# Kernel tuning notes

Hardware: AMD Instinct MI355X
Metric: run time of the kernel (lower is better)

The kernel has to match this reference:

```python
import jax, jax.numpy as jnp
import numpy as np

N = 50000
E = 1600000
IN, HID, OUT = 32, 64, 64

def setup_inputs() -> dict:
    key = jax.random.key(0)
    ks = jax.random.split(key, 10)
    x1 = jax.random.normal(ks[0], (N, IN), dtype=jnp.float32)
    x2 = jax.random.normal(ks[1], (N, IN), dtype=jnp.float32)
    ei1 = jax.random.randint(ks[2], (2, E), 0, N, dtype=jnp.int64)
    ei2 = jax.random.randint(ks[3], (2, E), 0, N, dtype=jnp.int64)
    s1 = 1.0 / np.sqrt(2 * IN)
    s2 = 1.0 / np.sqrt(2 * HID)
    W1 = jax.random.uniform(ks[4], (2 * IN, HID), jnp.float32, -s1, s1)
    b1 = jax.random.uniform(ks[5], (HID,), jnp.float32, -s1, s1)
    prelu_a = jnp.full((HID,), 0.25, dtype=jnp.float32)  # PReLU per-channel init
    W2 = jax.random.uniform(ks[6], (2 * HID, OUT), jnp.float32, -s2, s2)
    b2 = jax.random.uniform(ks[7], (OUT,), jnp.float32, -s2, s2)
    return {"x1": x1, "edge_index1": ei1, "x2": x2, "edge_index2": ei2,
            "W1": W1, "b1": b1, "prelu_a": prelu_a, "W2": W2, "b2": b2}

def _edge_conv(x, src, dst, W, b, n_nodes):
    # PyG EdgeConv: msg = MLP([x_i, x_j - x_i]), aggr = max over incoming edges
    xi = x[dst]                     # [E, d] target node feats
    xj = x[src]                     # [E, d] source node feats
    msg = jax.nn.relu(jnp.concatenate([xi, xj - xi], axis=-1) @ W + b)  # [E, out]
    agg = jax.ops.segment_max(msg, dst, num_segments=n_nodes)
    return jnp.where(jnp.isfinite(agg), agg, 0.0)  # nodes with no in-edges -> 0

def _prelu(x, a):
    return jnp.where(x >= 0, x, a * x)

def _embed(x, edge_index, W1, b1, prelu_a, W2, b2):
    src, dst = edge_index[0], edge_index[1]
    h = _prelu(_edge_conv(x, src, dst, W1, b1, x.shape[0]), prelu_a)
    return _edge_conv(h, src, dst, W2, b2, x.shape[0])

def reference(x1, edge_index1, x2, edge_index2, W1, b1, prelu_a, W2, b2):
    e1 = _embed(x1, edge_index1, W1, b1, prelu_a, W2, b2)
    e2 = _embed(x2, edge_index2, W1, b1, prelu_a, W2, b2)
    return (e1, e2)
```

## Files before the change

### kernel.cpp

```cpp
#include <hip/hip_runtime.h>
#include <hip/hip_fp16.h>


constexpr int HID   = 64;
constexpr int TILE  = 32;
constexpr int TSH   = 5;
constexpr int CAP   = 2048;
constexpr int MAXNB = 2048;
constexpr int EPT   = 16;
constexpr int CAPN  = 96;

typedef _Float16 half8 __attribute__((ext_vector_type(8)));
typedef float    f32x4 __attribute__((ext_vector_type(4)));

__device__ __forceinline__ unsigned int pkmax(unsigned int a, unsigned int b) {
    unsigned int d;
    asm("v_pk_max_f16 %0, %1, %2" : "=v"(d) : "v"(a), "v"(b));
    return d;
}
__device__ __forceinline__ unsigned int f2hbits(float f) {
    const __half h = __float2half_rn(f);
    return (unsigned int)*reinterpret_cast<const unsigned short*>(&h);
}
__device__ __forceinline__ float h2f(unsigned int b16) {
    const unsigned short b = (unsigned short)b16;
    __half h;
    *reinterpret_cast<unsigned short*>(&h) = b;
    return __half2float(h);
}

struct G {
    const float* x;
    const int*   src;
    const int*   dst;
    int* bcnt;
    unsigned int* bin;
    float*          u;
    unsigned short* vk;
    float*          out;
};

__global__ __launch_bounds__(256) void prep_w_kernel(
    const float* __restrict__ W1, const float* __restrict__ W2,
    _Float16* __restrict__ Wc1, _Float16* __restrict__ Wc2)
{
    const int i = blockIdx.x * 256 + threadIdx.x;
    if (i < 32 * 64) {
        const int k = i >> 6, c = i & 63;
        const float lo = W1[k * 64 + c], hi = W1[(32 + k) * 64 + c];
        Wc1[k * 128 + c]      = (_Float16)(lo - hi);
        Wc1[k * 128 + 64 + c] = (_Float16)hi;
    }
    const int j = i - 32 * 64;
    if (j >= 0 && j < 64 * 64) {
        const int k = j >> 6, c = j & 63;
        const float lo = W2[k * 64 + c], hi = W2[(64 + k) * 64 + c];
        Wc2[k * 128 + c]      = (_Float16)(lo - hi);
        Wc2[k * 128 + 64 + c] = (_Float16)hi;
    }
}

__global__ __launch_bounds__(256) void bin_kernel(G g0, G g1, int E, int NB) {
    const G g = blockIdx.y ? g1 : g0;
    __shared__ int lh[MAXNB];
    __shared__ int lb[MAXNB];
    for (int i = threadIdx.x; i < NB; i += 256) lh[i] = 0;
    __syncthreads();

    const int base = blockIdx.x * 256 * EPT;
    unsigned int rec[EPT];
    int bb[EPT];
    #pragma unroll
    for (int k = 0; k < EPT; ++k) {
        const int i = base + k * 256 + threadIdx.x;
        if (i < E) {
            const int d = g.dst[i];
            const int s = g.src[i];
            rec[k] = ((unsigned int)s << TSH) | (unsigned int)(d & (TILE - 1));
            bb[k]  = d >> TSH;
            atomicAdd(&lh[bb[k]], 1);
        } else bb[k] = -1;
    }
    __syncthreads();
    for (int t = threadIdx.x; t < NB; t += 256) {
        const int c = lh[t];
        lb[t] = c ? atomicAdd(&g.bcnt[t], c) : 0;
        lh[t] = 0;
    }
    __syncthreads();
    #pragma unroll
    for (int k = 0; k < EPT; ++k) {
        if (bb[k] >= 0) {
            const int off = atomicAdd(&lh[bb[k]], 1);
            const int pos = lb[bb[k]] + off;
            if (pos < CAP)
                g.bin[(size_t)bb[k] * CAP + pos] = rec[k];
        }
    }
}

template<int K>
__global__ __launch_bounds__(256) void gemm_mfma_kernel(
    G g0, G g1, const _Float16* __restrict__ Wc,
    const float* __restrict__ bias, int N)
{
    const G g = blockIdx.y ? g1 : g0;
    constexpr int KH = K / 32;
    const int lane = threadIdx.x & 63;
    const int m    = lane & 15;
    const int quad = lane >> 4;
    const int wid  = (blockIdx.x * 256 + threadIdx.x) >> 6;
    const int nW   = (gridDim.x * 256) >> 6;

    half8 bf[8][KH];
    #pragma unroll
    for (int t = 0; t < 8; ++t)
        #pragma unroll
        for (int h = 0; h < KH; ++h)
            #pragma unroll
            for (int j = 0; j < 8; ++j)
                bf[t][h][j] = Wc[(h * 32 + quad * 8 + j) * 128 + t * 16 + m];

    float bv[4];
    #pragma unroll
    for (int t = 0; t < 4; ++t) bv[t] = bias[t * 16 + m];

    const float* __restrict__ inp = (K == 32) ? g.x : g.out;
    const int tiles = (N + 15) / 16;

    for (int tile = wid; tile < tiles; tile += nW) {
        const int nbase = tile * 16;
        const int nodeA = min(nbase + m, N - 1);
        const float4* rp = (const float4*)(inp + (size_t)nodeA * K);

        half8 a[KH];
        #pragma unroll
        for (int h = 0; h < KH; ++h) {
            const float4 f0 = rp[h * 8 + quad * 2];
            const float4 f1 = rp[h * 8 + quad * 2 + 1];
            a[h][0] = (_Float16)f0.x; a[h][1] = (_Float16)f0.y;
            a[h][2] = (_Float16)f0.z; a[h][3] = (_Float16)f0.w;
            a[h][4] = (_Float16)f1.x; a[h][5] = (_Float16)f1.y;
            a[h][6] = (_Float16)f1.z; a[h][7] = (_Float16)f1.w;
        }

        f32x4 acc[8];
        #pragma unroll
        for (int t = 0; t < 8; ++t) {
            acc[t] = (f32x4){0.f, 0.f, 0.f, 0.f};
            #pragma unroll
            for (int h = 0; h < KH; ++h)
                acc[t] = __builtin_amdgcn_mfma_f32_16x16x32_f16(
                    a[h], bf[t][h], acc[t], 0, 0, 0);
        }

        #pragma unroll
        for (int r = 0; r < 4; ++r) {
            const int node = nbase + quad * 4 + r;
            if (node < N) {
                float* urow = g.u + (size_t)node * HID;
                #pragma unroll
                for (int t = 0; t < 4; ++t)
                    urow[t * 16 + m] = acc[t][r] + bv[t];
                const unsigned int e0 = f2hbits(acc[4][r]);
                const unsigned int e1 = f2hbits(acc[5][r]);
                const unsigned int e2 = f2hbits(acc[6][r]);
                const unsigned int e3 = f2hbits(acc[7][r]);
                uint2 pack;
                pack.x = (e1 << 16) | e0;
                pack.y = (e3 << 16) | e2;
                ((uint2*)(g.vk + (size_t)node * HID))[m] = pack;
            }
        }
    }
}

__global__ __launch_bounds__(256) void agg_kernel(G g0, G g1, int N, int NB, int two) {
    int b, gi;
    if (two) {
        const int bid = blockIdx.x;
        const int xcd = bid & 7;
        gi = xcd >> 2;
        b  = (bid >> 3) * 4 + (xcd & 3);
    } else { gi = 0; b = blockIdx.x; }
    if (b >= NB) return;
    const G g = gi ? g1 : g0;

    __shared__ int lcnt[TILE];
    __shared__ unsigned short lrec[TILE][CAPN];
    for (int i = threadIdx.x; i < TILE; i += 256) lcnt[i] = 0;
    __syncthreads();

    const int cnt = min(g.bcnt[b], CAP);
    const unsigned int* __restrict__ bp = g.bin + (size_t)b * CAP;
    for (int i = threadIdx.x; i < cnt; i += 256) {
        const unsigned int rec = bp[i];
        const int d = rec & (TILE - 1);
        const int p = atomicAdd(&lcnt[d], 1);
        if (p < CAPN) lrec[d][p] = (unsigned short)(rec >> TSH);
    }
    __syncthreads();

    const int grp = threadIdx.x >> 4;
    const int sub = threadIdx.x & 15;
    const uint2* __restrict__ vk2 = (const uint2*)g.vk;

    #pragma unroll
    for (int half = 0; half < 2; ++half) {
        const int nl = grp + half * 16;
        const int n  = b * TILE + nl;
        if (n >= N) continue;
        const int c = min(lcnt[nl], CAPN);

        unsigned int m0 = 0xFC00FC00u, m1 = 0xFC00FC00u;
        int j = 0;
        for (; j + 8 <= c; j += 8) {
            const uint4 rq = *(const uint4*)(&lrec[nl][j]);
            unsigned int s[8];
            s[0] = rq.x & 0xFFFFu; s[1] = rq.x >> 16;
            s[2] = rq.y & 0xFFFFu; s[3] = rq.y >> 16;
            s[4] = rq.z & 0xFFFFu; s[5] = rq.z >> 16;
            s[6] = rq.w & 0xFFFFu; s[7] = rq.w >> 16;
            uint2 a[8];
            #pragma unroll
            for (int k = 0; k < 8; ++k) a[k] = vk2[(size_t)s[k] * 16 + sub];
            #pragma unroll
            for (int k = 0; k < 8; ++k) {
                m0 = pkmax(m0, a[k].x);
                m1 = pkmax(m1, a[k].y);
            }
        }
        for (; j < c; ++j) {
            const uint2 a = vk2[(size_t)lrec[nl][j] * 16 + sub];
            m0 = pkmax(m0, a.x);
            m1 = pkmax(m1, a.y);
        }

        float mv[4];
        mv[0] = h2f(m0 & 0xFFFFu); mv[1] = h2f(m0 >> 16);
        mv[2] = h2f(m1 & 0xFFFFu); mv[3] = h2f(m1 >> 16);

        const float* __restrict__ urow = g.u + (size_t)n * HID;
        float* __restrict__ orow = g.out + (size_t)n * HID;
        #pragma unroll
        for (int t = 0; t < 4; ++t) {
            float r = 0.f;
            if (c > 0) r = fmaxf(urow[sub + 16 * t] + mv[t], 0.f);
            orow[sub + 16 * t] = r;
        }
    }
}


extern "C" void kernel_launch(void* const* d_in, const int* in_sizes, int n_in,
                              void* d_out, int out_size, void* d_ws, size_t ws_size,
                              hipStream_t stream) {
    const float* x1  = (const float*)d_in[0];
    const int*   ei1 = (const int*)d_in[1];
    const float* x2  = (const float*)d_in[2];
    const int*   ei2 = (const int*)d_in[3];
    const float* W1  = (const float*)d_in[4];
    const float* b1  = (const float*)d_in[5];
    const float* W2  = (const float*)d_in[7];
    const float* b2  = (const float*)d_in[8];

    const int N  = in_sizes[0] / 32;
    const int E  = in_sizes[1] / 2;
    const int NB = (N + TILE - 1) / TILE;
    float* out = (float*)d_out;

    const size_t rowB = (size_t)N * HID * sizeof(float);
    const size_t vkB  = ((size_t)N * HID * 2 + 63) & ~(size_t)63;
    const size_t binB = ((size_t)NB * CAP * sizeof(int) + 63) & ~(size_t)63;
    const size_t nbB  = ((size_t)(NB + 2) * sizeof(int) + 63) & ~(size_t)63;
    const size_t wc1B = ((size_t)32 * 128 * 2 + 63) & ~(size_t)63;
    const size_t wc2B = ((size_t)64 * 128 * 2 + 63) & ~(size_t)63;

    const int bBlk = (E + 256 * EPT - 1) / (256 * EPT);
    const int gBlk = 256;
    const int pBlk = (32 * 64 + 64 * 64 + 255) / 256;
    const int aggBlk2 = ((NB + 3) / 4) * 8;

    _Float16* wc1 = nullptr;
    _Float16* wc2 = nullptr;

    auto run = [&](G ga, G gb, int ny) {
        hipMemsetAsync(ga.bcnt, 0, (size_t)ny * nbB, stream);
        bin_kernel <<<dim3(bBlk, ny), 256, 0, stream>>>(ga, gb, E, NB);
        gemm_mfma_kernel<32><<<dim3(gBlk, ny), 256, 0, stream>>>(ga, gb, wc1, b1, N);
        if (ny == 2) agg_kernel<<<aggBlk2, 256, 0, stream>>>(ga, gb, N, NB, 1);
        else         agg_kernel<<<NB,      256, 0, stream>>>(ga, ga, N, NB, 0);
        gemm_mfma_kernel<64><<<dim3(gBlk, ny), 256, 0, stream>>>(ga, gb, wc2, b2, N);
        if (ny == 2) agg_kernel<<<aggBlk2, 256, 0, stream>>>(ga, gb, N, NB, 1);
        else         agg_kernel<<<NB,      256, 0, stream>>>(ga, ga, N, NB, 0);
    };

    char* ws = (char*)d_ws;
    const size_t needBoth = 2 * rowB + 2 * vkB + 2 * binB + 2 * nbB + wc1B + wc2B;

    if (ws_size >= needBoth) {
        float* u0 = (float*)ws;                  ws += rowB;
        float* u1 = (float*)ws;                  ws += rowB;
        unsigned int* bin0 = (unsigned int*)ws;  ws += binB;
        unsigned int* bin1 = (unsigned int*)ws;  ws += binB;
        unsigned short* vk0 = (unsigned short*)ws;  ws += vkB;
        unsigned short* vk1 = (unsigned short*)ws;  ws += vkB;
        wc1 = (_Float16*)ws;                     ws += wc1B;
        wc2 = (_Float16*)ws;                     ws += wc2B;
        int* bcnt0 = (int*)ws;                   ws += nbB;
        int* bcnt1 = (int*)ws;

        G g0{x1, ei1, ei1 + E, bcnt0, bin0, u0, vk0, out};
        G g1{x2, ei2, ei2 + E, bcnt1, bin1, u1, vk1, out + (size_t)N * HID};
        prep_w_kernel<<<pBlk, 256, 0, stream>>>(W1, W2, wc1, wc2);
        run(g0, g1, 2);
    } else {
        float* u = (float*)ws;                   ws += rowB;
        unsigned int* bin = (unsigned int*)ws;   ws += binB;
        unsigned short* vk = (unsigned short*)ws;  ws += vkB;
        wc1 = (_Float16*)ws;                     ws += wc1B;
        wc2 = (_Float16*)ws;                     ws += wc2B;
        int* bcnt = (int*)ws;

        prep_w_kernel<<<pBlk, 256, 0, stream>>>(W1, W2, wc1, wc2);
        for (int g = 0; g < 2; ++g) {
            const int* ei = g ? ei2 : ei1;
            G gp{g ? x2 : x1, ei, ei + E, bcnt, bin,
                 u, vk, out + (size_t)g * N * HID};
            run(gp, gp, 1);
        }
    }
}
```

Measured before the change: 249.2 us.

## Widen agg tiles to 128 nodes with sentinel-padded edge lists and split halves

The node tile grows from 32 to 128 per block, and bin capacity and the number of buckets change to match. Each node's incoming edge list is padded to a multiple of 8 using a sentinel row N, which prep_w_kernel fills with -inf fp16, so the scalar tail loop is gone. Each 8-lane group now handles four nodes in two passes, one per column half, which raises loads in flight per thread. The cost is larger shared-memory tiles, extra gathers of the sentinel row, and fewer, heavier blocks. It also relies on N fitting in 16 bits and on CAP=5120 being enough per 128-node bin.

Measured after the change: 299.7 us. +20.3%, slower.

```diff
diff --git a/kernel.cpp b/kernel.cpp
--- a/kernel.cpp
+++ b/kernel.cpp
@@ -3,10 +3,10 @@
 
 
 constexpr int HID   = 64;
-constexpr int TILE  = 32;
-constexpr int TSH   = 5;
-constexpr int CAP   = 2048;
-constexpr int MAXNB = 2048;
+constexpr int TILE  = 128;
+constexpr int TSH   = 7;
+constexpr int CAP   = 5120;
+constexpr int MAXNB = 512;
 constexpr int EPT   = 16;
 constexpr int CAPN  = 96;
 
@@ -42,7 +42,8 @@
 
 __global__ __launch_bounds__(256) void prep_w_kernel(
     const float* __restrict__ W1, const float* __restrict__ W2,
-    _Float16* __restrict__ Wc1, _Float16* __restrict__ Wc2)
+    _Float16* __restrict__ Wc1, _Float16* __restrict__ Wc2,
+    unsigned short* __restrict__ vkS0, unsigned short* __restrict__ vkS1, int N)
 {
     const int i = blockIdx.x * 256 + threadIdx.x;
     if (i < 32 * 64) {
@@ -57,6 +58,11 @@
         const float lo = W2[k * 64 + c], hi = W2[(64 + k) * 64 + c];
         Wc2[k * 128 + c]      = (_Float16)(lo - hi);
         Wc2[k * 128 + 64 + c] = (_Float16)hi;
+    }
+    const int q = i - (32 * 64 + 64 * 64);
+    if (q >= 0 && q < 2 * HID) {
+        if (q < HID) vkS0[(size_t)N * HID + q]       = 0xFC00u;
+        else         vkS1[(size_t)N * HID + (q-HID)] = 0xFC00u;
     }
 }
 
@@ -200,21 +206,27 @@
         if (p < CAPN) lrec[d][p] = (unsigned short)(rec >> TSH);
     }
     __syncthreads();
-
-    const int grp = threadIdx.x >> 4;
-    const int sub = threadIdx.x & 15;
+    for (int t = threadIdx.x; t < TILE; t += 256) {
+        const int c  = min(lcnt[t], CAPN);
+        const int cp = (c + 7) & ~7;
+        for (int p = c; p < cp; ++p) lrec[t][p] = (unsigned short)N;
+        lcnt[t] = cp;
+    }
+    __syncthreads();
+
+    const int grp = threadIdx.x >> 3;
+    const int sub = threadIdx.x & 7;
     const uint2* __restrict__ vk2 = (const uint2*)g.vk;
 
-    #pragma unroll
-    for (int half = 0; half < 2; ++half) {
-        const int nl = grp + half * 16;
-        const int n  = b * TILE + nl;
-        if (n >= N) continue;
-        const int c = min(lcnt[nl], CAPN);
-
+    unsigned int mA[4][2], mB[4][2];
+    int cp4[4];
+
+    #pragma unroll
+    for (int i = 0; i < 4; ++i) {
+        const int nl = grp + 32 * i;
+        cp4[i] = lcnt[nl];
         unsigned int m0 = 0xFC00FC00u, m1 = 0xFC00FC00u;
-        int j = 0;
-        for (; j + 8 <= c; j += 8) {
+        for (int j = 0; j < cp4[i]; j += 8) {
             const uint4 rq = *(const uint4*)(&lrec[nl][j]);
             unsigned int s[8];
             s[0] = rq.x & 0xFFFFu; s[1] = rq.x >> 16;
@@ -230,24 +242,47 @@
                 m1 = pkmax(m1, a[k].y);
             }
         }
-        for (; j < c; ++j) {
-            const uint2 a = vk2[(size_t)lrec[nl][j] * 16 + sub];
-            m0 = pkmax(m0, a.x);
-            m1 = pkmax(m1, a.y);
-        }
-
-        float mv[4];
-        mv[0] = h2f(m0 & 0xFFFFu); mv[1] = h2f(m0 >> 16);
-        mv[2] = h2f(m1 & 0xFFFFu); mv[3] = h2f(m1 >> 16);
-
+        mA[i][0] = m0; mA[i][1] = m1;
+    }
+
+    #pragma unroll
+    for (int i = 0; i < 4; ++i) {
+        const int nl = grp + 32 * i;
+        unsigned int m0 = 0xFC00FC00u, m1 = 0xFC00FC00u;
+        for (int j = 0; j < cp4[i]; j += 8) {
+            const uint4 rq = *(const uint4*)(&lrec[nl][j]);
+            unsigned int s[8];
+            s[0] = rq.x & 0xFFFFu; s[1] = rq.x >> 16;
+            s[2] = rq.y & 0xFFFFu; s[3] = rq.y >> 16;
+            s[4] = rq.z & 0xFFFFu; s[5] = rq.z >> 16;
+            s[6] = rq.w & 0xFFFFu; s[7] = rq.w >> 16;
+            uint2 a[8];
+            #pragma unroll
+            for (int k = 0; k < 8; ++k) a[k] = vk2[(size_t)s[k] * 16 + 8 + sub];
+            #pragma unroll
+            for (int k = 0; k < 8; ++k) {
+                m0 = pkmax(m0, a[k].x);
+                m1 = pkmax(m1, a[k].y);
+            }
+        }
+        mB[i][0] = m0; mB[i][1] = m1;
+    }
+
+    #pragma unroll
+    for (int i = 0; i < 4; ++i) {
+        const int nl = grp + 32 * i;
+        const int n  = b * TILE + nl;
+        if (n >= N) continue;
+        const bool has = cp4[i] > 0;
         const float* __restrict__ urow = g.u + (size_t)n * HID;
         float* __restrict__ orow = g.out + (size_t)n * HID;
-        #pragma unroll
-        for (int t = 0; t < 4; ++t) {
-            float r = 0.f;
-            if (c > 0) r = fmaxf(urow[sub + 16 * t] + mv[t], 0.f);
-            orow[sub + 16 * t] = r;
-        }
+        #define PUT(C, HW) \
+            orow[C] = has ? fmaxf(urow[C] + h2f(HW), 0.f) : 0.f;
+        PUT(sub,      mA[i][0] & 0xFFFFu)  PUT(sub + 16, mA[i][0] >> 16)
+        PUT(sub + 32, mA[i][1] & 0xFFFFu)  PUT(sub + 48, mA[i][1] >> 16)
+        PUT(sub + 8,  mB[i][0] & 0xFFFFu)  PUT(sub + 24, mB[i][0] >> 16)
+        PUT(sub + 40, mB[i][1] & 0xFFFFu)  PUT(sub + 56, mB[i][1] >> 16)
+        #undef PUT
     }
 }
 
@@ -270,7 +305,7 @@
     float* out = (float*)d_out;
 
     const size_t rowB = (size_t)N * HID * sizeof(float);
-    const size_t vkB  = ((size_t)N * HID * 2 + 63) & ~(size_t)63;
+    const size_t vkB  = ((size_t)(N + 1) * HID * 2 + 63) & ~(size_t)63;
     const size_t binB = ((size_t)NB * CAP * sizeof(int) + 63) & ~(size_t)63;
     const size_t nbB  = ((size_t)(NB + 2) * sizeof(int) + 63) & ~(size_t)63;
     const size_t wc1B = ((size_t)32 * 128 * 2 + 63) & ~(size_t)63;
@@ -278,7 +313,7 @@
 
     const int bBlk = (E + 256 * EPT - 1) / (256 * EPT);
     const int gBlk = 256;
-    const int pBlk = (32 * 64 + 64 * 64 + 255) / 256;
+    const int pBlk = (32 * 64 + 64 * 64 + 2 * HID + 255) / 256;
     const int aggBlk2 = ((NB + 3) / 4) * 8;
 
     _Float16* wc1 = nullptr;
@@ -312,7 +347,7 @@
 
         G g0{x1, ei1, ei1 + E, bcnt0, bin0, u0, vk0, out};
         G g1{x2, ei2, ei2 + E, bcnt1, bin1, u1, vk1, out + (size_t)N * HID};
-        prep_w_kernel<<<pBlk, 256, 0, stream>>>(W1, W2, wc1, wc2);
+        prep_w_kernel<<<pBlk, 256, 0, stream>>>(W1, W2, wc1, wc2, vk0, vk1, N);
         run(g0, g1, 2);
     } else {
         float* u = (float*)ws;                   ws += rowB;
@@ -322,7 +357,7 @@
         wc2 = (_Float16*)ws;                     ws += wc2B;
         int* bcnt = (int*)ws;
 
-        prep_w_kernel<<<pBlk, 256, 0, stream>>>(W1, W2, wc1, wc2);
+        prep_w_kernel<<<pBlk, 256, 0, stream>>>(W1, W2, wc1, wc2, vk, vk, N);
         for (int g = 0; g < 2; ++g) {
             const int* ei = g ? ei2 : ei1;
             G gp{g ? x2 : x1, ei, ei + E, bcnt, bin,
```

## Bin edges into 128-node tiles, split aggregation in halves, pad neighbor lists with sentinel

Applied to the files above, without the earlier changes.

Edges are now binned into 128-node tiles with larger per-bin capacity, and each agg block handles one 64-node half of a tile. The block filters the shared bin by half and processes four node groups per thread group. Neighbor lists are padded to a multiple of 8 with a sentinel row N whose vk entries are preset to -inf fp16, which removes the scalar tail loop. The change is meant to cut bin-kernel atomics and histogram size and to keep the 8-wide gather loop branch-free. In exchange, each bin is read twice (once per half), bin capacity may overflow, and the gemm grid size also changes.

New measurement: 264.3 us. +6.0%, slower.

```diff
diff --git a/kernel.cpp b/kernel.cpp
--- a/kernel.cpp
+++ b/kernel.cpp
@@ -3,11 +3,12 @@
 
 
 constexpr int HID   = 64;
-constexpr int TILE  = 32;
-constexpr int TSH   = 5;
-constexpr int CAP   = 2048;
-constexpr int MAXNB = 2048;
-constexpr int EPT   = 16;
+constexpr int TILE  = 128;
+constexpr int TSH   = 7;
+constexpr int HTILE = 64;
+constexpr int CAP   = 5120;
+constexpr int MAXNB = 512;
+constexpr int EPT   = 8;
 constexpr int CAPN  = 96;
 
 typedef _Float16 half8 __attribute__((ext_vector_type(8)));
@@ -42,7 +43,8 @@
 
 __global__ __launch_bounds__(256) void prep_w_kernel(
     const float* __restrict__ W1, const float* __restrict__ W2,
-    _Float16* __restrict__ Wc1, _Float16* __restrict__ Wc2)
+    _Float16* __restrict__ Wc1, _Float16* __restrict__ Wc2,
+    unsigned short* __restrict__ vkS0, unsigned short* __restrict__ vkS1, int N)
 {
     const int i = blockIdx.x * 256 + threadIdx.x;
     if (i < 32 * 64) {
@@ -57,6 +59,11 @@
         const float lo = W2[k * 64 + c], hi = W2[(64 + k) * 64 + c];
         Wc2[k * 128 + c]      = (_Float16)(lo - hi);
         Wc2[k * 128 + 64 + c] = (_Float16)hi;
+    }
+    const int q = i - (32 * 64 + 64 * 64);
+    if (q >= 0 && q < 2 * HID) {
+        if (q < HID) vkS0[(size_t)N * HID + q]       = 0xFC00u;
+        else         vkS1[(size_t)N * HID + (q-HID)] = 0xFC00u;
     }
 }
 
@@ -176,28 +183,40 @@
 }
 
 __global__ __launch_bounds__(256) void agg_kernel(G g0, G g1, int N, int NB, int two) {
-    int b, gi;
+    int idx, gi;
     if (two) {
         const int bid = blockIdx.x;
         const int xcd = bid & 7;
-        gi = xcd >> 2;
-        b  = (bid >> 3) * 4 + (xcd & 3);
-    } else { gi = 0; b = blockIdx.x; }
-    if (b >= NB) return;
+        gi  = xcd >> 2;
+        idx = (bid >> 3) * 4 + (xcd & 3);
+    } else { gi = 0; idx = blockIdx.x; }
+    if (idx >= 2 * NB) return;
+    const int b    = idx >> 1;
+    const int half = idx & 1;
     const G g = gi ? g1 : g0;
 
-    __shared__ int lcnt[TILE];
-    __shared__ unsigned short lrec[TILE][CAPN];
-    for (int i = threadIdx.x; i < TILE; i += 256) lcnt[i] = 0;
-    __syncthreads();
-
-    const int cnt = min(g.bcnt[b], CAP);
+    __shared__ int lcnt[HTILE];
+    __shared__ unsigned short lrec[HTILE][CAPN];
+    for (int i = threadIdx.x; i < HTILE; i += 256) lcnt[i] = 0;
+    __syncthreads();
+
+    const int cnt  = min(g.bcnt[b], CAP);
+    const int hsel = half << 6;
     const unsigned int* __restrict__ bp = g.bin + (size_t)b * CAP;
     for (int i = threadIdx.x; i < cnt; i += 256) {
         const unsigned int rec = bp[i];
         const int d = rec & (TILE - 1);
-        const int p = atomicAdd(&lcnt[d], 1);
-        if (p < CAPN) lrec[d][p] = (unsigned short)(rec >> TSH);
+        if ((d & 64) == hsel) {
+            const int p = atomicAdd(&lcnt[d & 63], 1);
+            if (p < CAPN) lrec[d & 63][p] = (unsigned short)(rec >> TSH);
+        }
+    }
+    __syncthreads();
+    for (int t = threadIdx.x; t < HTILE; t += 256) {
+        const int c  = min(lcnt[t], CAPN);
+        const int cp = (c + 7) & ~7;
+        for (int p = c; p < cp; ++p) lrec[t][p] = (unsigned short)N;
+        lcnt[t] = cp;
     }
     __syncthreads();
 
@@ -206,15 +225,14 @@
     const uint2* __restrict__ vk2 = (const uint2*)g.vk;
 
     #pragma unroll
-    for (int half = 0; half < 2; ++half) {
-        const int nl = grp + half * 16;
-        const int n  = b * TILE + nl;
+    for (int i = 0; i < 4; ++i) {
+        const int nl = grp + 16 * i;
+        const int n  = b * TILE + half * HTILE + nl;
         if (n >= N) continue;
-        const int c = min(lcnt[nl], CAPN);
+        const int cp = lcnt[nl];
 
         unsigned int m0 = 0xFC00FC00u, m1 = 0xFC00FC00u;
-        int j = 0;
-        for (; j + 8 <= c; j += 8) {
+        for (int j = 0; j < cp; j += 8) {
             const uint4 rq = *(const uint4*)(&lrec[nl][j]);
             unsigned int s[8];
             s[0] = rq.x & 0xFFFFu; s[1] = rq.x >> 16;
@@ -230,24 +248,18 @@
                 m1 = pkmax(m1, a[k].y);
             }
         }
-        for (; j < c; ++j) {
-            const uint2 a = vk2[(size_t)lrec[nl][j] * 16 + sub];
-            m0 = pkmax(m0, a.x);
-            m1 = pkmax(m1, a.y);
-        }
 
         float mv[4];
         mv[0] = h2f(m0 & 0xFFFFu); mv[1] = h2f(m0 >> 16);
         mv[2] = h2f(m1 & 0xFFFFu); mv[3] = h2f(m1 >> 16);
 
+        const bool has = cp > 0;
         const float* __restrict__ urow = g.u + (size_t)n * HID;
         float* __restrict__ orow = g.out + (size_t)n * HID;
         #pragma unroll
-        for (int t = 0; t < 4; ++t) {
-            float r = 0.f;
-            if (c > 0) r = fmaxf(urow[sub + 16 * t] + mv[t], 0.f);
-            orow[sub + 16 * t] = r;
-        }
+        for (int t = 0; t < 4; ++t)
+            orow[sub + 16 * t] =
+                has ? fmaxf(urow[sub + 16 * t] + mv[t], 0.f) : 0.f;
     }
 }
 
@@ -270,16 +282,17 @@
     float* out = (float*)d_out;
 
     const size_t rowB = (size_t)N * HID * sizeof(float);
-    const size_t vkB  = ((size_t)N * HID * 2 + 63) & ~(size_t)63;
+    const size_t vkB  = ((size_t)(N + 1) * HID * 2 + 63) & ~(size_t)63;
     const size_t binB = ((size_t)NB * CAP * sizeof(int) + 63) & ~(size_t)63;
     const size_t nbB  = ((size_t)(NB + 2) * sizeof(int) + 63) & ~(size_t)63;
     const size_t wc1B = ((size_t)32 * 128 * 2 + 63) & ~(size_t)63;
     const size_t wc2B = ((size_t)64 * 128 * 2 + 63) & ~(size_t)63;
 
     const int bBlk = (E + 256 * EPT - 1) / (256 * EPT);
-    const int gBlk = 256;
-    const int pBlk = (32 * 64 + 64 * 64 + 255) / 256;
-    const int aggBlk2 = ((NB + 3) / 4) * 8;
+    const int gBlk = 512;
+    const int pBlk = (32 * 64 + 64 * 64 + 2 * HID + 255) / 256;
+    const int aggBlk2 = ((2 * NB + 3) / 4) * 8;
+    const int aggBlk1 = 2 * NB;
 
     _Float16* wc1 = nullptr;
     _Float16* wc2 = nullptr;
@@ -289,10 +302,10 @@
         bin_kernel <<<dim3(bBlk, ny), 256, 0, stream>>>(ga, gb, E, NB);
         gemm_mfma_kernel<32><<<dim3(gBlk, ny), 256, 0, stream>>>(ga, gb, wc1, b1, N);
         if (ny == 2) agg_kernel<<<aggBlk2, 256, 0, stream>>>(ga, gb, N, NB, 1);
-        else         agg_kernel<<<NB,      256, 0, stream>>>(ga, ga, N, NB, 0);
+        else         agg_kernel<<<aggBlk1, 256, 0, stream>>>(ga, ga, N, NB, 0);
         gemm_mfma_kernel<64><<<dim3(gBlk, ny), 256, 0, stream>>>(ga, gb, wc2, b2, N);
         if (ny == 2) agg_kernel<<<aggBlk2, 256, 0, stream>>>(ga, gb, N, NB, 1);
-        else         agg_kernel<<<NB,      256, 0, stream>>>(ga, ga, N, NB, 0);
+        else         agg_kernel<<<aggBlk1, 256, 0, stream>>>(ga, ga, N, NB, 0);
     };
 
     char* ws = (char*)d_ws;
@@ -312,7 +325,7 @@
 
         G g0{x1, ei1, ei1 + E, bcnt0, bin0, u0, vk0, out};
         G g1{x2, ei2, ei2 + E, bcnt1, bin1, u1, vk1, out + (size_t)N * HID};
-        prep_w_kernel<<<pBlk, 256, 0, stream>>>(W1, W2, wc1, wc2);
+        prep_w_kernel<<<pBlk, 256, 0, stream>>>(W1, W2, wc1, wc2, vk0, vk1, N);
         run(g0, g1, 2);
     } else {
         float* u = (float*)ws;                   ws += rowB;
@@ -322,7 +335,7 @@
         wc2 = (_Float16*)ws;                     ws += wc2B;
         int* bcnt = (int*)ws;
 
-        prep_w_kernel<<<pBlk, 256, 0, stream>>>(W1, W2, wc1, wc2);
+        prep_w_kernel<<<pBlk, 256, 0, stream>>>(W1, W2, wc1, wc2, vk, vk, N);
         for (int g = 0; g < 2; ++g) {
             const int* ei = g ? ei2 : ei1;
             G gp{g ? x2 : x1, ei, ei + E, bcnt, bin,
```
